# Performance work log

Hardware: AMD Instinct MI355X
Metric: run time of the kernel (lower is better)

Reference implementation:

```python
import jax, jax.numpy as jnp
import numpy as np

K = 16  # k1: neighbors kept
D = 2   # d1: dilation


def setup_inputs() -> dict:
    key = jax.random.key(0)
    k1, k2 = jax.random.split(key)
    new_xyz = jax.random.normal(k1, (8, 4096, 3), dtype=jnp.float32)
    new_points = jax.random.normal(k2, (8, 4096, 64), dtype=jnp.float32)
    return {"new_xyz": new_xyz, "new_points": new_points}


def _dg_knn_idx(new_points):
    sq = jnp.sum(new_points * new_points, axis=-1)              # [B,N]
    inner = jnp.einsum('bnc,bmc->bnm', new_points, new_points)  # [B,N,N]
    adj = sq[:, :, None] - 2.0 * inner + sq[:, None, :]
    # dilated kNN: top (K*D) nearest, then stride by D
    _, idx = jax.lax.top_k(-adj, K * D)                         # [B,N,K*D]
    return idx[:, :, ::D]                                       # [B,N,K]


def reference(new_xyz, new_points):
    nn_idx = _dg_knn_idx(new_points)                            # [B,N,K] int32
    # index_points: gather neighbor coordinates -> [B,N,K,3]
    neighbor_xyz = jax.vmap(lambda pts, idx: pts[idx])(new_xyz, nn_idx)
    xyz_tile = jnp.broadcast_to(new_xyz[:, :, None, :], neighbor_xyz.shape)
    relative_xyz = xyz_tile - neighbor_xyz                      # [B,N,K,3]
    relative_dis = jnp.sqrt(jnp.sum(relative_xyz * relative_xyz, axis=-1, keepdims=True))
    # [B,N,K, 1+3+3+3] = [B,N,K,10]
    return jnp.concatenate([relative_dis, relative_xyz, xyz_tile, neighbor_xyz], axis=-1)
```

## Files before the change

kernel.cpp:

```cpp
#include <hip/hip_runtime.h>
#include <stdint.h>

typedef unsigned long long u64;
typedef __attribute__((ext_vector_type(8))) short s16x8;
typedef __attribute__((ext_vector_type(4))) float f32x4v;
typedef __attribute__((ext_vector_type(4))) unsigned int u32x4;
typedef __attribute__((ext_vector_type(2))) unsigned int u32x2;

#define NB 8
#define NPTS 4096
#define NC 64
#define KOUT 16
#define TSEL 36
#define CHUNK 64
#define NCHUNK (NPTS / CHUNK)
#define IDXBITS 0xFFFu
#define KEYMASK 0xFFFFF000u
#define RPW 4
#define RPB 16
#define ROWB 144

__global__ __launch_bounds__(256) void sq_kernel(const float* __restrict__ pts,
                                                 float* __restrict__ sqw) {
    int p = blockIdx.x * 256 + threadIdx.x;
    const float* r = pts + (size_t)p * NC;
    float acc[8];
#pragma unroll
    for (int j = 0; j < 8; ++j) acc[j] = __fmul_rn(r[j], r[j]);
#pragma unroll
    for (int i = 8; i < 64; i += 8)
#pragma unroll
        for (int j = 0; j < 8; ++j)
            acc[j] = __fadd_rn(acc[j], __fmul_rn(r[i + j], r[i + j]));
    float s01 = __fadd_rn(acc[0], acc[1]);
    float s23 = __fadd_rn(acc[2], acc[3]);
    float s45 = __fadd_rn(acc[4], acc[5]);
    float s67 = __fadd_rn(acc[6], acc[7]);
    sqw[p] = __fadd_rn(__fadd_rn(s01, s23), __fadd_rn(s45, s67));
}

static __device__ __forceinline__ uint32_t pkbf(float a, float b) {
#if __has_builtin(__builtin_amdgcn_perm)
    return __builtin_amdgcn_perm(__float_as_uint(b), __float_as_uint(a), 0x07060302);
#else
    return (__float_as_uint(b) & 0xFFFF0000u) | (__float_as_uint(a) >> 16);
#endif
}

__device__ __forceinline__ void stream_insert(uint32_t& list, uint32_t cand, int lane) {
    uint32_t thr = (uint32_t)__builtin_amdgcn_readlane((int)list, TSEL - 1);
    u64 mask = __ballot(cand < thr);
    while (mask) {
        int src = __ffsll((long long)mask) - 1;
        uint32_t v = (uint32_t)__builtin_amdgcn_readlane((int)cand, src);
        int pos = __popcll(__ballot(list < v));
        uint32_t up = __shfl_up(list, 1);
        list = (lane < pos) ? list : ((lane == pos) ? v : up);
        mask &= (mask - 1);
    }
}

__device__ __forceinline__ void epilogue(uint32_t list, int n, int b, int lane,
                                         const float* __restrict__ pb,
                                         const float* __restrict__ sqb,
                                         float sqn,
                                         const float* __restrict__ xyz,
                                         float* __restrict__ out) {
    int m = (int)(list & IDXBITS);
    const float4* xr = (const float4*)(pb + (size_t)n * NC);
    const float4* yr = (const float4*)(pb + (size_t)m * NC);
    float acc = 0.f;
#pragma unroll
    for (int i = 0; i < 16; ++i) {
        float4 xv = xr[i];
        float4 yv = yr[i];
        acc = __fmaf_rn(xv.x, yv.x, acc);
        acc = __fmaf_rn(xv.y, yv.y, acc);
        acc = __fmaf_rn(xv.z, yv.z, acc);
        acc = __fmaf_rn(xv.w, yv.w, acc);
    }
    float key = __fadd_rn(__fsub_rn(sqn, __fmul_rn(2.0f, acc)), sqb[m]);

    int rank = 0;
    uint32_t kb = __float_as_uint(key);
#pragma unroll 1
    for (int j = 0; j < TSEL; ++j) {
        float kj = __uint_as_float(
            (uint32_t)__builtin_amdgcn_readlane((int)kb, j));
        int mj = __builtin_amdgcn_readlane(m, j);
        bool less = (kj < key) || (kj == key && mj < m);
        rank += less ? 1 : 0;
    }
    if (lane < TSEL && rank < 2 * KOUT && (rank & 1) == 0) {
        int k = rank >> 1;
        const float* xn = xyz + ((size_t)b * NPTS + n) * 3;
        const float* xm = xyz + ((size_t)b * NPTS + m) * 3;
        float xnx = xn[0], xny = xn[1], xnz = xn[2];
        float ox = xm[0], oy = xm[1], oz = xm[2];
        float rx = xnx - ox, ry = xny - oy, rz = xnz - oz;
        float dis = sqrtf(rx * rx + ry * ry + rz * rz);
        float* o = out + (((size_t)b * NPTS + n) * KOUT + k) * 10;
        o[0] = dis; o[1] = rx; o[2] = ry; o[3] = rz;
        o[4] = xnx; o[5] = xny; o[6] = xnz;
        o[7] = ox;  o[8] = oy;  o[9] = oz;
    }
}

__global__ __launch_bounds__(256, 3) void knn_kernel(
    const float* __restrict__ xyz,
    const float* __restrict__ pts,
    const float* __restrict__ sqw,
    float* __restrict__ out) {

    __shared__ __align__(16) unsigned short ylds[2][CHUNK * (ROWB / 2)];
    __shared__ __align__(16) float slds[2][4][16][20];

    const int tid = threadIdx.x;
    const int lane = tid & 63;
    const int wave = tid >> 6;
    const int b = blockIdx.x >> 8;
    const int rowbase = (blockIdx.x & 255) << 4;
    const int nw = __builtin_amdgcn_readfirstlane(rowbase + wave * RPW);
    const float* pb = pts + (size_t)b * NPTS * NC;
    const float* sqb = sqw + (size_t)b * NPTS;

    s16x8 afrag0, afrag1;
    {
        const float* xrow = pb + (size_t)(rowbase + (lane & 15)) * NC + (lane >> 4) * 8;
        float4 xa0 = *(const float4*)(xrow);
        float4 xa1 = *(const float4*)(xrow + 4);
        float4 xb0 = *(const float4*)(xrow + 32);
        float4 xb1 = *(const float4*)(xrow + 36);
        u32x4 a0p = { pkbf(xa0.x, xa0.y), pkbf(xa0.z, xa0.w),
                      pkbf(xa1.x, xa1.y), pkbf(xa1.z, xa1.w) };
        u32x4 a1p = { pkbf(xb0.x, xb0.y), pkbf(xb0.z, xb0.w),
                      pkbf(xb1.x, xb1.y), pkbf(xb1.z, xb1.w) };
        afrag0 = __builtin_bit_cast(s16x8, a0p);
        afrag1 = __builtin_bit_cast(s16x8, a1p);
    }

    float sqn[RPW];
#pragma unroll
    for (int r = 0; r < RPW; ++r) sqn[r] = sqb[nw + r];

    uint32_t list[RPW];
#pragma unroll
    for (int r = 0; r < RPW; ++r) list[r] = 0xFFFFFFFFu;

    const float4* gsrc = (const float4*)pb;
    float4 pf[4];
#pragma unroll
    for (int j = 0; j < 4; ++j) pf[j] = gsrc[tid + 256 * j];

#pragma unroll
    for (int j = 0; j < 4; ++j) {
        int s = tid + 256 * j;
        u32x2 w2 = { pkbf(pf[j].x, pf[j].y), pkbf(pf[j].z, pf[j].w) };
        *(u32x2*)((char*)ylds[0] + (s >> 4) * ROWB + (s & 15) * 8) = w2;
    }
    __syncthreads();

    for (int c = 0; c < NCHUNK; ++c) {
        const int cb = c & 1;
        if (c + 1 < NCHUNK) {
#pragma unroll
            for (int j = 0; j < 4; ++j)
                pf[j] = gsrc[(size_t)(c + 1) * (CHUNK * 16) + tid + 256 * j];
        }
        const int m = c * CHUNK + lane;
        float sqm = sqb[m];
        {
            const char* bp = (const char*)ylds[cb] + wave * (16 * ROWB)
                           + (lane & 15) * ROWB + (lane >> 4) * 16;
            s16x8 b0 = *(const s16x8*)(bp);
            s16x8 b1 = *(const s16x8*)(bp + 64);
            f32x4v cc = {0.f, 0.f, 0.f, 0.f};
            cc = __builtin_amdgcn_mfma_f32_16x16x32_bf16(afrag0, b0, cc, 0, 0, 0);
            cc = __builtin_amdgcn_mfma_f32_16x16x32_bf16(afrag1, b1, cc, 0, 0, 0);
            *(f32x4v*)&slds[cb][wave][lane & 15][(lane >> 4) * 4] = cc;
        }
        if (c + 1 < NCHUNK) {
#pragma unroll
            for (int j = 0; j < 4; ++j) {
                int s = tid + 256 * j;
                u32x2 w2 = { pkbf(pf[j].x, pf[j].y), pkbf(pf[j].z, pf[j].w) };
                *(u32x2*)((char*)ylds[cb ^ 1] + (s >> 4) * ROWB + (s & 15) * 8) = w2;
            }
        }
        __syncthreads();
        {
            f32x4v ip = *(const f32x4v*)&slds[cb][lane >> 4][lane & 15][wave * 4];
            float ipr[RPW] = { ip.x, ip.y, ip.z, ip.w };
#pragma unroll
            for (int r = 0; r < RPW; ++r) {
                float t = fmaxf(fmaf(-2.f, ipr[r], sqn[r] + sqm), 0.f);
                uint32_t cd = (__float_as_uint(t) & KEYMASK) | (unsigned)m;
                stream_insert(list[r], cd, lane);
            }
        }
    }

#pragma unroll 1
    for (int r = 0; r < RPW; ++r)
        epilogue(list[r], nw + r, b, lane, pb, sqb, sqn[r], xyz, out);
}

extern "C" void kernel_launch(void* const* d_in, const int* in_sizes, int n_in,
                              void* d_out, int out_size, void* d_ws, size_t ws_size,
                              hipStream_t stream) {
    const float* xyz = (const float*)d_in[0];
    const float* pts = (const float*)d_in[1];
    float* sqw = (float*)d_ws;
    float* out = (float*)d_out;

    sq_kernel<<<(NB * NPTS) / 256, 256, 0, stream>>>(pts, sqw);
    knn_kernel<<<(NB * NPTS) / RPB, 256, 0, stream>>>(xyz, pts, sqw, out);
}
```

Before: 351.5 us.

## Precompute swizzled bf16 points and stream chunks into LDS with async global_load_lds

New measurement: 348.9 us. Within noise of the previous version (-0.7%).

```diff
diff --git a/kernel.cpp b/kernel.cpp
--- a/kernel.cpp
+++ b/kernel.cpp
@@ -20,6 +20,12 @@
 #define RPB 16
 #define ROWB 144
 
+typedef const void __attribute__((address_space(1))) cvg_t;
+typedef void __attribute__((address_space(3))) vl_t;
+static __device__ __forceinline__ void async16(const void* g, void* l) {
+    __builtin_amdgcn_global_load_lds((cvg_t*)g, (vl_t*)l, 16, 0, 0);
+}
+
 __global__ __launch_bounds__(256) void sq_kernel(const float* __restrict__ pts,
                                                  float* __restrict__ sqw) {
     int p = blockIdx.x * 256 + threadIdx.x;
@@ -45,6 +51,16 @@
 #else
     return (__float_as_uint(b) & 0xFFFF0000u) | (__float_as_uint(a) >> 16);
 #endif
+}
+
+__global__ __launch_bounds__(256) void cvt_kernel(const float* __restrict__ pts,
+                                                  uint32_t* __restrict__ bfw) {
+    int t = blockIdx.x * 256 + threadIdx.x;
+    int p = t >> 5;
+    int q = t & 31;
+    int j = ((((q >> 2) ^ (p & 7)) << 2) | (q & 3));
+    const float* r = pts + (size_t)p * NC + 2 * j;
+    bfw[(size_t)p * 32 + q] = pkbf(r[0], r[1]);
 }
 
 __device__ __forceinline__ void stream_insert(uint32_t& list, uint32_t cand, int lane) {
@@ -106,13 +122,15 @@
     }
 }
 
+template<bool PRE>
 __global__ __launch_bounds__(256, 3) void knn_kernel(
     const float* __restrict__ xyz,
     const float* __restrict__ pts,
     const float* __restrict__ sqw,
+    const unsigned short* __restrict__ bfw,
     float* __restrict__ out) {
 
-    __shared__ __align__(16) unsigned short ylds[2][CHUNK * (ROWB / 2)];
+    __shared__ __align__(16) unsigned short ylds[2][CHUNK * (PRE ? 64 : 72)];
     __shared__ __align__(16) float slds[2][4][16][20];
 
     const int tid = threadIdx.x;
@@ -148,43 +166,67 @@
     for (int r = 0; r < RPW; ++r) list[r] = 0xFFFFFFFFu;
 
     const float4* gsrc = (const float4*)pb;
+    const char* gbf = (const char*)(bfw + (size_t)b * NPTS * NC);
     float4 pf[4];
-#pragma unroll
-    for (int j = 0; j < 4; ++j) pf[j] = gsrc[tid + 256 * j];
-
-#pragma unroll
-    for (int j = 0; j < 4; ++j) {
-        int s = tid + 256 * j;
-        u32x2 w2 = { pkbf(pf[j].x, pf[j].y), pkbf(pf[j].z, pf[j].w) };
-        *(u32x2*)((char*)ylds[0] + (s >> 4) * ROWB + (s & 15) * 8) = w2;
+
+    if constexpr (PRE) {
+        async16(gbf + tid * 16, (char*)ylds[0] + tid * 16);
+        async16(gbf + 4096 + tid * 16, (char*)ylds[0] + 4096 + tid * 16);
+    } else {
+#pragma unroll
+        for (int j = 0; j < 4; ++j) pf[j] = gsrc[tid + 256 * j];
+#pragma unroll
+        for (int j = 0; j < 4; ++j) {
+            int s = tid + 256 * j;
+            u32x2 w2 = { pkbf(pf[j].x, pf[j].y), pkbf(pf[j].z, pf[j].w) };
+            *(u32x2*)((char*)ylds[0] + (s >> 4) * ROWB + (s & 15) * 8) = w2;
+        }
     }
     __syncthreads();
 
     for (int c = 0; c < NCHUNK; ++c) {
         const int cb = c & 1;
         if (c + 1 < NCHUNK) {
-#pragma unroll
-            for (int j = 0; j < 4; ++j)
-                pf[j] = gsrc[(size_t)(c + 1) * (CHUNK * 16) + tid + 256 * j];
+            if constexpr (PRE) {
+                const char* gs = gbf + (size_t)(c + 1) * (CHUNK * NC * 2);
+                char* lb = (char*)ylds[cb ^ 1];
+                async16(gs + tid * 16, lb + tid * 16);
+                async16(gs + 4096 + tid * 16, lb + 4096 + tid * 16);
+            } else {
+#pragma unroll
+                for (int j = 0; j < 4; ++j)
+                    pf[j] = gsrc[(size_t)(c + 1) * (CHUNK * 16) + tid + 256 * j];
+            }
         }
         const int m = c * CHUNK + lane;
         float sqm = sqb[m];
         {
-            const char* bp = (const char*)ylds[cb] + wave * (16 * ROWB)
-                           + (lane & 15) * ROWB + (lane >> 4) * 16;
-            s16x8 b0 = *(const s16x8*)(bp);
-            s16x8 b1 = *(const s16x8*)(bp + 64);
+            s16x8 b0, b1;
+            if constexpr (PRE) {
+                const char* yb = (const char*)ylds[cb] + wave * (16 * 128)
+                               + (lane & 15) * 128;
+                const int bx = lane & 7;
+                b0 = *(const s16x8*)(yb + ((((lane >> 4)    ) ^ bx) << 4));
+                b1 = *(const s16x8*)(yb + ((((lane >> 4) + 4) ^ bx) << 4));
+            } else {
+                const char* bp = (const char*)ylds[cb] + wave * (16 * ROWB)
+                               + (lane & 15) * ROWB + (lane >> 4) * 16;
+                b0 = *(const s16x8*)(bp);
+                b1 = *(const s16x8*)(bp + 64);
+            }
             f32x4v cc = {0.f, 0.f, 0.f, 0.f};
             cc = __builtin_amdgcn_mfma_f32_16x16x32_bf16(afrag0, b0, cc, 0, 0, 0);
             cc = __builtin_amdgcn_mfma_f32_16x16x32_bf16(afrag1, b1, cc, 0, 0, 0);
             *(f32x4v*)&slds[cb][wave][lane & 15][(lane >> 4) * 4] = cc;
         }
-        if (c + 1 < NCHUNK) {
-#pragma unroll
-            for (int j = 0; j < 4; ++j) {
-                int s = tid + 256 * j;
-                u32x2 w2 = { pkbf(pf[j].x, pf[j].y), pkbf(pf[j].z, pf[j].w) };
-                *(u32x2*)((char*)ylds[cb ^ 1] + (s >> 4) * ROWB + (s & 15) * 8) = w2;
+        if constexpr (!PRE) {
+            if (c + 1 < NCHUNK) {
+#pragma unroll
+                for (int j = 0; j < 4; ++j) {
+                    int s = tid + 256 * j;
+                    u32x2 w2 = { pkbf(pf[j].x, pf[j].y), pkbf(pf[j].z, pf[j].w) };
+                    *(u32x2*)((char*)ylds[cb ^ 1] + (s >> 4) * ROWB + (s & 15) * 8) = w2;
+                }
             }
         }
         __syncthreads();
@@ -214,5 +256,13 @@
     float* out = (float*)d_out;
 
     sq_kernel<<<(NB * NPTS) / 256, 256, 0, stream>>>(pts, sqw);
-    knn_kernel<<<(NB * NPTS) / RPB, 256, 0, stream>>>(xyz, pts, sqw, out);
-}
+
+    const size_t need = 32768 * sizeof(float) + (size_t)NB * NPTS * NC * 2;
+    if (ws_size >= need) {
+        unsigned short* bfw = (unsigned short*)((char*)d_ws + 32768 * sizeof(float));
+        cvt_kernel<<<(NB * NPTS * 32) / 256, 256, 0, stream>>>(pts, (uint32_t*)bfw);
+        knn_kernel<true><<<(NB * NPTS) / RPB, 256, 0, stream>>>(xyz, pts, sqw, bfw, out);
+    } else {
+        knn_kernel<false><<<(NB * NPTS) / RPB, 256, 0, stream>>>(xyz, pts, sqw, nullptr, out);
+    }
+}
```
